# Performance work log

Hardware: AMD Instinct MI355X
Metric: run time of the kernel (lower is better)

Reference implementation:

```python
import jax, jax.numpy as jnp
import numpy as np

B, T, H, W, D = 64, 512, 768, 256, 256  # batch, tokens, bert hidden, max words, embedding_dim


def setup_inputs() -> dict:
    key = jax.random.key(0)
    k1, k2, k3 = jax.random.split(key, 3)
    hidden_states = jax.random.normal(k1, (B, T, H), dtype=jnp.float32)
    # word_ids from a fast tokenizer are nondecreasing within a sentence
    word_ids = jnp.sort(jax.random.randint(k2, (B, T), 0, W), axis=-1)
    proj_w = jax.random.normal(k3, (H, D), dtype=jnp.float32) / np.sqrt(H).astype(np.float32)
    proj_b = jnp.zeros((D,), dtype=jnp.float32)
    return {"hidden_states": hidden_states, "word_ids": word_ids,
            "proj_w": proj_w, "proj_b": proj_b}


def _segment_mean(h, wid):
    # h: [T, H], wid: [T]. Invalid ids (<0 or >=W, i.e. special/pad tokens)
    # are routed to a dump segment W that is sliced away.
    idx = jnp.where((wid >= 0) & (wid < W), wid, W)
    sums = jax.ops.segment_sum(h, idx, num_segments=W + 1)[:W]          # [W, H]
    counts = jax.ops.segment_sum(jnp.ones((h.shape[0],), h.dtype), idx,
                                 num_segments=W + 1)[:W]                 # [W]
    # torch.clamp(counts, min=1) -> padded/empty words stay zero
    return sums / jnp.maximum(counts, 1.0)[:, None]


def reference(hidden_states, word_ids, proj_w, proj_b):
    # token-to-word scatter-mean pooling, vectorized over batch
    word_emb = jax.vmap(_segment_mean)(hidden_states, word_ids)  # [B, W, H]
    # final linear projection to embedding_dim
    return jnp.einsum('bwh,hd->bwd', word_emb, proj_w) + proj_b  # [B, W, D]
```

## Files before the change

### kernel.cpp

```cpp
#include <hip/hip_runtime.h>


#define NB 64
#define NT 512
#define NH 768
#define NW 256
#define ND 256
#define PAD 8
#define ROWE (NH + PAD)

typedef __attribute__((ext_vector_type(8))) short short8;
typedef __attribute__((ext_vector_type(4))) float f32x4;
typedef __attribute__((ext_vector_type(4))) float float4v;
typedef __attribute__((ext_vector_type(4))) unsigned short ushort4v;

__device__ __forceinline__ unsigned short f2bf(float f) {
    union { float f; unsigned u; } v; v.f = f;
    unsigned r = v.u + 0x7fffu + ((v.u >> 16) & 1u);
    return (unsigned short)(r >> 16);
}

__global__ void prep_wt2(const float* __restrict__ w, unsigned short* __restrict__ wt2) {
    __shared__ float tile[32][33];
    const int tid = threadIdx.x, n = blockIdx.x;
    const int tx = tid & 31, ty = tid >> 5;
    const int k0 = (n % 24) * 32, n0 = (n / 24) * 32;
    #pragma unroll
    for (int i = 0; i < 4; ++i)
        tile[ty + 8 * i][tx] = w[(size_t)(k0 + ty + 8 * i) * ND + n0 + tx];
    __syncthreads();
    if (tid < 128) {
        const int cc = tid & 31, q = tid >> 5;
        const int col = n0 + cc;
        ushort4v u0, u1;
        #pragma unroll
        for (int j = 0; j < 4; ++j) u0[j] = f2bf(tile[q * 8 + j][cc]);
        #pragma unroll
        for (int j = 0; j < 4; ++j) u1[j] = f2bf(tile[q * 8 + 4 + j][cc]);
        size_t off = (((size_t)(col >> 4) * 96 + (k0 >> 3) + q) * 16 + (col & 15)) * 8;
        *(ushort4v*)&wt2[off]     = u0;
        *(ushort4v*)&wt2[off + 4] = u1;
    }
}

__device__ __forceinline__ void pool4(const int* __restrict__ sb, int wi,
                                      unsigned short (*__restrict__ At)[ROWE], int rr,
                                      const float* __restrict__ base, int lane) {
    const int s0 = sb[wi],     s1 = sb[wi + 1];
    const int s2 = sb[wi + 2], s3 = sb[wi + 3];
    const int s4 = sb[wi + 4];

    float4v acc[4][3];
    #pragma unroll
    for (int r = 0; r < 4; ++r)
        #pragma unroll
        for (int c = 0; c < 3; ++c)
            #pragma unroll
            for (int q = 0; q < 4; ++q) acc[r][c][q] = 0.f;

#define ADD3_(ar, vv) { _Pragma("unroll")                                     \
        for (int q = 0; q < 4; ++q) {                                         \
            ar[0][q] += (vv)[0][q]; ar[1][q] += (vv)[1][q]; ar[2][q] += (vv)[2][q]; } }
#define ROUTE4_(tt, vv) {                                                     \
        if ((tt) < s1)      { ADD3_(acc[0], vv); }                            \
        else if ((tt) < s2) { ADD3_(acc[1], vv); }                            \
        else if ((tt) < s3) { ADD3_(acc[2], vv); }                            \
        else                { ADD3_(acc[3], vv); } }

    int t = s0;
    for (; t + 4 <= s4; t += 4) {
        float4v v[4][3];
        #pragma unroll
        for (int u = 0; u < 4; ++u) {
            const float* p2 = base + (size_t)(t + u) * NH;
            v[u][0] = *(const float4v*)(p2);
            v[u][1] = *(const float4v*)(p2 + 256);
            v[u][2] = *(const float4v*)(p2 + 512);
        }
        #pragma unroll
        for (int u = 0; u < 4; ++u) ROUTE4_(t + u, v[u]);
    }
    for (; t < s4; ++t) {
        float4v v1[3];
        const float* p2 = base + (size_t)t * NH;
        v1[0] = *(const float4v*)(p2);
        v1[1] = *(const float4v*)(p2 + 256);
        v1[2] = *(const float4v*)(p2 + 512);
        ROUTE4_(t, v1);
    }
#undef ROUTE4_
#undef ADD3_

    #pragma unroll
    for (int r = 0; r < 4; ++r) {
        int cs = (r == 0) ? s0 : (r == 1) ? s1 : (r == 2) ? s2 : s3;
        int ce = (r == 0) ? s1 : (r == 1) ? s2 : (r == 2) ? s3 : s4;
        int cnt = ce - cs; if (cnt < 1) cnt = 1;
        const float sc = 1.0f / (float)cnt;
        #pragma unroll
        for (int c = 0; c < 3; ++c) {
            ushort4v u;
            #pragma unroll
            for (int q = 0; q < 4; ++q) u[q] = f2bf(acc[r][c][q] * sc);
            *(ushort4v*)&At[rr + r][c * 256 + lane * 4] = u;
        }
    }
}

__global__ __launch_bounds__(512, 2)
void fused(const float* __restrict__ hs, const int* __restrict__ wid,
           const unsigned short* __restrict__ wt2, const float* __restrict__ pb,
           float* __restrict__ out) {
    __shared__ unsigned short A0t[32][ROWE];
    __shared__ unsigned short A1t[32][ROWE];
    __shared__ int swid[NT];
    __shared__ int sb[65];

    const int tid = threadIdx.x, bid = blockIdx.x;
    const int wave = tid >> 6, lane = tid & 63;
    const int b = bid >> 2, W0 = (bid & 3) * 64;

    swid[tid] = wid[b * NT + tid];
    __syncthreads();
    if (tid <= 64) {
        int v = W0 + tid, lo = 0, hi = NT;
        while (lo < hi) { int mid = (lo + hi) >> 1; if (swid[mid] < v) lo = mid + 1; else hi = mid; }
        sb[tid] = lo;
    }
    __syncthreads();

    const float* base = hs + (size_t)b * NT * NH + lane * 4;
    const int cl = lane & 15, kg = lane >> 4;

    pool4(sb, wave * 4, A0t, wave * 4, base, lane);
    __syncthreads();

    if (wave < 4) {
        const int c0w = wave * 64;
        const unsigned short* bgp = wt2 + (size_t)(wave * 4) * 12288 + kg * 128 + cl * 8;
        short8 a0[2], a1[2], b0[4], b1[4];
        f32x4 acc[2][4];
        #pragma unroll
        for (int mt = 0; mt < 2; ++mt)
            #pragma unroll
            for (int nt = 0; nt < 4; ++nt)
                #pragma unroll
                for (int r = 0; r < 4; ++r) acc[mt][nt][r] = 0.f;

#define LDA0(d, ks) { d[0] = *(const short8*)&A0t[cl][(ks) * 32 + kg * 8];    \
                      d[1] = *(const short8*)&A0t[16 + cl][(ks) * 32 + kg * 8]; }
#define LDB0(d, ks) { _Pragma("unroll")                                       \
                      for (int nt = 0; nt < 4; ++nt)                          \
                          d[nt] = *(const short8*)(bgp + nt * 12288 + (ks) * 512); }
#define MM0(a, bb) { _Pragma("unroll")                                        \
                     for (int mt = 0; mt < 2; ++mt)                           \
                         _Pragma("unroll")                                    \
                         for (int nt = 0; nt < 4; ++nt)                       \
                             acc[mt][nt] = __builtin_amdgcn_mfma_f32_16x16x32_bf16(a[mt], bb[nt], acc[mt][nt], 0, 0, 0); }

        LDA0(a0, 0); LDB0(b0, 0);
        #pragma unroll 1
        for (int i = 0; i < 12; ++i) {
            const int ks = 2 * i;
            LDA0(a1, ks + 1); LDB0(b1, ks + 1);
            MM0(a0, b0);
            if (i < 11) { LDA0(a0, ks + 2); LDB0(b0, ks + 2); }
            MM0(a1, b1);
        }
#undef LDA0
#undef LDB0
#undef MM0

        float bv[4];
        #pragma unroll
        for (int nt = 0; nt < 4; ++nt) bv[nt] = pb[c0w + nt * 16 + cl];

        #pragma unroll
        for (int mt = 0; mt < 2; ++mt)
            #pragma unroll
            for (int nt = 0; nt < 4; ++nt)
                #pragma unroll
                for (int r = 0; r < 4; ++r)
                    out[((size_t)b * NW + W0 + mt * 16 + kg * 4 + r) * ND + c0w + nt * 16 + cl]
                        = acc[mt][nt][r] + bv[nt];
    } else {
        const int wv = wave - 4;
        pool4(sb, 32 + wv * 8,     A1t, wv * 8,     base, lane);
        pool4(sb, 32 + wv * 8 + 4, A1t, wv * 8 + 4, base, lane);
    }
    __syncthreads();

    {
        const int c0w = wave * 32;
        const unsigned short* bgp = wt2 + (size_t)(wave * 2) * 12288 + kg * 128 + cl * 8;
        short8 a0f[2], a1f[2], b0f[2], b1f[2];
        f32x4 acc[2][2];
        #pragma unroll
        for (int mt = 0; mt < 2; ++mt)
            #pragma unroll
            for (int nt = 0; nt < 2; ++nt)
                #pragma unroll
                for (int r = 0; r < 4; ++r) acc[mt][nt][r] = 0.f;

#define LDA1(d, ks) { d[0] = *(const short8*)&A1t[cl][(ks) * 32 + kg * 8];    \
                      d[1] = *(const short8*)&A1t[16 + cl][(ks) * 32 + kg * 8]; }
#define LDB1(d, ks) { _Pragma("unroll")                                       \
                      for (int nt = 0; nt < 2; ++nt)                          \
                          d[nt] = *(const short8*)(bgp + nt * 12288 + (ks) * 512); }
#define MM1(a, bb) { _Pragma("unroll")                                        \
                     for (int mt = 0; mt < 2; ++mt)                           \
                         _Pragma("unroll")                                    \
                         for (int nt = 0; nt < 2; ++nt)                       \
                             acc[mt][nt] = __builtin_amdgcn_mfma_f32_16x16x32_bf16(a[mt], bb[nt], acc[mt][nt], 0, 0, 0); }

        LDA1(a0f, 0); LDB1(b0f, 0);
        #pragma unroll 1
        for (int i = 0; i < 12; ++i) {
            const int ks = 2 * i;
            LDA1(a1f, ks + 1); LDB1(b1f, ks + 1);
            MM1(a0f, b0f);
            if (i < 11) { LDA1(a0f, ks + 2); LDB1(b0f, ks + 2); }
            MM1(a1f, b1f);
        }
#undef LDA1
#undef LDB1
#undef MM1

        float bv[2];
        bv[0] = pb[c0w + cl];
        bv[1] = pb[c0w + 16 + cl];

        #pragma unroll
        for (int mt = 0; mt < 2; ++mt)
            #pragma unroll
            for (int nt = 0; nt < 2; ++nt)
                #pragma unroll
                for (int r = 0; r < 4; ++r)
                    out[((size_t)b * NW + W0 + 32 + mt * 16 + kg * 4 + r) * ND + c0w + nt * 16 + cl]
                        = acc[mt][nt][r] + bv[nt];
    }
}

extern "C" void kernel_launch(void* const* d_in, const int* in_sizes, int n_in,
                              void* d_out, int out_size, void* d_ws, size_t ws_size,
                              hipStream_t stream) {
    const float* hs  = (const float*)d_in[0];
    const int*   wid = (const int*)d_in[1];
    const float* pw  = (const float*)d_in[2];
    const float* pb  = (const float*)d_in[3];
    float* out = (float*)d_out;

    unsigned short* wt2 = (unsigned short*)d_ws;

    prep_wt2<<<192, 256, 0, stream>>>(pw, wt2);
    fused<<<NB * 4, 512, 0, stream>>>(hs, wid, wt2, pb, out);
}
```

Before: 34.42 us.

## Rebalance second-half pooling between GEMM waves and pooling waves

Pooling of the second 32-word half is no longer done only by waves 4-7 (8 words each). Those waves now pool 6 words each, and waves 0-3 pool 2 words each after finishing their first-half GEMM. A templated poolW<W> with predicated per-segment routing replaces the fixed 4-word pool function. The aim is to shorten the critical path of the phase where GEMM and pooling overlap. The cost is extra compare/branch work per token in the generic routing.

```diff
diff --git a/kernel.cpp b/kernel.cpp
--- a/kernel.cpp
+++ b/kernel.cpp
@@ -43,32 +43,25 @@
     }
 }
 
-__device__ __forceinline__ void pool4(const int* __restrict__ sb, int wi,
+template<int W>
+__device__ __forceinline__ void poolW(const int* __restrict__ sbp,
                                       unsigned short (*__restrict__ At)[ROWE], int rr,
                                       const float* __restrict__ base, int lane) {
-    const int s0 = sb[wi],     s1 = sb[wi + 1];
-    const int s2 = sb[wi + 2], s3 = sb[wi + 3];
-    const int s4 = sb[wi + 4];
-
-    float4v acc[4][3];
-    #pragma unroll
-    for (int r = 0; r < 4; ++r)
+    int s[W + 1];
+    #pragma unroll
+    for (int i = 0; i <= W; ++i) s[i] = sbp[i];
+
+    float4v acc[W][3];
+    #pragma unroll
+    for (int r = 0; r < W; ++r)
         #pragma unroll
         for (int c = 0; c < 3; ++c)
             #pragma unroll
             for (int q = 0; q < 4; ++q) acc[r][c][q] = 0.f;
 
-#define ADD3_(ar, vv) { _Pragma("unroll")                                     \
-        for (int q = 0; q < 4; ++q) {                                         \
-            ar[0][q] += (vv)[0][q]; ar[1][q] += (vv)[1][q]; ar[2][q] += (vv)[2][q]; } }
-#define ROUTE4_(tt, vv) {                                                     \
-        if ((tt) < s1)      { ADD3_(acc[0], vv); }                            \
-        else if ((tt) < s2) { ADD3_(acc[1], vv); }                            \
-        else if ((tt) < s3) { ADD3_(acc[2], vv); }                            \
-        else                { ADD3_(acc[3], vv); } }
-
-    int t = s0;
-    for (; t + 4 <= s4; t += 4) {
+    int t = s[0];
+    const int tend = s[W];
+    for (; t + 4 <= tend; t += 4) {
         float4v v[4][3];
         #pragma unroll
         for (int u = 0; u < 4; ++u) {
@@ -78,24 +71,40 @@
             v[u][2] = *(const float4v*)(p2 + 512);
         }
         #pragma unroll
-        for (int u = 0; u < 4; ++u) ROUTE4_(t + u, v[u]);
-    }
-    for (; t < s4; ++t) {
-        float4v v1[3];
+        for (int u = 0; u < 4; ++u) {
+            const int tt = t + u;
+            #pragma unroll
+            for (int r = 0; r < W; ++r)
+                if (tt >= s[r] && tt < s[r + 1]) {
+                    #pragma unroll
+                    for (int q = 0; q < 4; ++q) {
+                        acc[r][0][q] += v[u][0][q];
+                        acc[r][1][q] += v[u][1][q];
+                        acc[r][2][q] += v[u][2][q];
+                    }
+                }
+        }
+    }
+    for (; t < tend; ++t) {
         const float* p2 = base + (size_t)t * NH;
-        v1[0] = *(const float4v*)(p2);
-        v1[1] = *(const float4v*)(p2 + 256);
-        v1[2] = *(const float4v*)(p2 + 512);
-        ROUTE4_(t, v1);
-    }
-#undef ROUTE4_
-#undef ADD3_
-
-    #pragma unroll
-    for (int r = 0; r < 4; ++r) {
-        int cs = (r == 0) ? s0 : (r == 1) ? s1 : (r == 2) ? s2 : s3;
-        int ce = (r == 0) ? s1 : (r == 1) ? s2 : (r == 2) ? s3 : s4;
-        int cnt = ce - cs; if (cnt < 1) cnt = 1;
+        float4v v0 = *(const float4v*)(p2);
+        float4v v1 = *(const float4v*)(p2 + 256);
+        float4v v2 = *(const float4v*)(p2 + 512);
+        #pragma unroll
+        for (int r = 0; r < W; ++r)
+            if (t >= s[r] && t < s[r + 1]) {
+                #pragma unroll
+                for (int q = 0; q < 4; ++q) {
+                    acc[r][0][q] += v0[q];
+                    acc[r][1][q] += v1[q];
+                    acc[r][2][q] += v2[q];
+                }
+            }
+    }
+
+    #pragma unroll
+    for (int r = 0; r < W; ++r) {
+        int cnt = s[r + 1] - s[r]; if (cnt < 1) cnt = 1;
         const float sc = 1.0f / (float)cnt;
         #pragma unroll
         for (int c = 0; c < 3; ++c) {
@@ -132,7 +141,7 @@
     const float* base = hs + (size_t)b * NT * NH + lane * 4;
     const int cl = lane & 15, kg = lane >> 4;
 
-    pool4(sb, wave * 4, A0t, wave * 4, base, lane);
+    poolW<4>(&sb[wave * 4], A0t, wave * 4, base, lane);
     __syncthreads();
 
     if (wave < 4) {
@@ -183,10 +192,11 @@
                 for (int r = 0; r < 4; ++r)
                     out[((size_t)b * NW + W0 + mt * 16 + kg * 4 + r) * ND + c0w + nt * 16 + cl]
                         = acc[mt][nt][r] + bv[nt];
+
+        poolW<2>(&sb[56 + 2 * wave], A1t, 24 + 2 * wave, base, lane);
     } else {
         const int wv = wave - 4;
-        pool4(sb, 32 + wv * 8,     A1t, wv * 8,     base, lane);
-        pool4(sb, 32 + wv * 8 + 4, A1t, wv * 8 + 4, base, lane);
+        poolW<6>(&sb[32 + wv * 6], A1t, wv * 6, base, lane);
     }
     __syncthreads();
 
```

Measured after the change: 36.15 us. 1.05x slower.
